# Optimization experiments

Hardware: AMD Instinct MI355X
Metric: run time of the kernel (lower is better)

Reference implementation:

```python
import jax, jax.numpy as jnp
import numpy as np

N, D_FEAT, D, H, L = 2048, 128, 256, 8, 2
DH = D // H
E = 65536
NUM_EDGE_TYPES = 8
MAX_DIST = 10
MAX_DEGREE = 512
D_FF = 4 * D
D_OUT = 128
EPS = 1e-5


def _layernorm(x, g, b):
    mu = jnp.mean(x, axis=-1, keepdims=True)
    var = jnp.mean(jnp.square(x - mu), axis=-1, keepdims=True)
    return (x - mu) * jax.lax.rsqrt(var + EPS) * g + b


def setup_inputs() -> dict:
    key = jax.random.key(0)
    ks = jax.random.split(key, 32)
    inp = {
        "x": jax.random.normal(ks[0], (N, D_FEAT), dtype=jnp.float32),
        "edge_index": jax.random.randint(ks[1], (2, E), 0, N),
        "edge_types": jax.random.randint(ks[2], (E,), 0, NUM_EDGE_TYPES),
        "pos_encoding": jax.random.uniform(ks[3], (N, N), dtype=jnp.float32),
    }
    def xavier(k, shape):
        fan_in, fan_out = shape[0], shape[1]
        lim = float(np.sqrt(6.0 / (fan_in + fan_out)))
        return jax.random.uniform(k, shape, jnp.float32, -lim, lim)
    inp["W_emb"] = xavier(ks[4], (D_FEAT, D)); inp["b_emb"] = jnp.zeros((D,), jnp.float32)
    # stacked per-layer params, stored as [in, out] so y = x @ W + b
    inp["Wq"] = jnp.stack([xavier(jax.random.fold_in(ks[5], l), (D, D)) for l in range(L)])
    inp["Wk"] = jnp.stack([xavier(jax.random.fold_in(ks[6], l), (D, D)) for l in range(L)])
    inp["Wv"] = jnp.stack([xavier(jax.random.fold_in(ks[7], l), (D, D)) for l in range(L)])
    inp["Wo"] = jnp.stack([xavier(jax.random.fold_in(ks[8], l), (D, D)) for l in range(L)])
    for nm in ("bq", "bk", "bv", "bo"):
        inp[nm] = jnp.zeros((L, D), jnp.float32)
    inp["spd_table"] = 0.02 * jax.random.normal(ks[9], (L, MAX_DIST + 1, H), dtype=jnp.float32)
    inp["edge_table"] = 0.02 * jax.random.normal(ks[10], (L, NUM_EDGE_TYPES, H), dtype=jnp.float32)
    inp["din_emb"] = 0.02 * jax.random.normal(ks[11], (L, MAX_DEGREE + 1, D), dtype=jnp.float32)
    inp["dout_emb"] = 0.02 * jax.random.normal(ks[12], (L, MAX_DEGREE + 1, D), dtype=jnp.float32)
    inp["ln1_g"] = jnp.ones((L, D), jnp.float32); inp["ln1_b"] = jnp.zeros((L, D), jnp.float32)
    inp["ln2_g"] = jnp.ones((L, D), jnp.float32); inp["ln2_b"] = jnp.zeros((L, D), jnp.float32)
    inp["W1"] = jnp.stack([xavier(jax.random.fold_in(ks[13], l), (D, D_FF)) for l in range(L)])
    inp["b1"] = jnp.zeros((L, D_FF), jnp.float32)
    inp["W2"] = jnp.stack([xavier(jax.random.fold_in(ks[14], l), (D_FF, D)) for l in range(L)])
    inp["b2"] = jnp.zeros((L, D), jnp.float32)
    inp["W_out"] = xavier(ks[15], (D, D_OUT)); inp["b_out"] = jnp.zeros((D_OUT,), jnp.float32)
    return inp


def _forward(x, edge_index, edge_types, pos_encoding,
             W_emb, b_emb, Wq, bq, Wk, bk, Wv, bv, Wo, bo,
             spd_table, edge_table, din_emb, dout_emb,
             ln1_g, ln1_b, ln2_g, ln2_b, W1, b1, W2, b2, W_out, b_out):
    src, dst = edge_index[0], edge_index[1]
    ones = jnp.ones((E,), jnp.int32)
    deg_out = jnp.clip(jax.ops.segment_sum(ones, src, num_segments=N), 0, MAX_DEGREE)
    deg_in = jnp.clip(jax.ops.segment_sum(ones, dst, num_segments=N), 0, MAX_DEGREE)
    # SPD bucket matrix [N, N] (int), shared across layers
    spd_bucket = jnp.clip(pos_encoding[:, :N] * MAX_DIST + 0.5, 0, MAX_DIST).astype(jnp.int32)

    h = x @ W_emb + b_emb  # node embedding; dropout=0 (eval)
    scale = 1.0 / np.sqrt(DH)
    for l in range(L):
        # centrality encoding
        h = h + din_emb[l][deg_in] + dout_emb[l][deg_out]
        xn = _layernorm(h, ln1_g[l], ln1_b[l])
        q = (xn @ Wq[l] + bq[l]).reshape(N, H, DH).transpose(1, 0, 2)  # [H,N,DH]
        k = (xn @ Wk[l] + bk[l]).reshape(N, H, DH).transpose(1, 0, 2)
        v = (xn @ Wv[l] + bv[l]).reshape(N, H, DH).transpose(1, 0, 2)
        # attention bias [H, N, N]: SPD table gather + per-edge scatter-add
        bias = spd_table[l][spd_bucket].transpose(2, 0, 1)
        e_bias = edge_table[l][edge_types]  # [E, H]
        bias = bias.at[:, src, dst].add(e_bias.T)
        scores = jnp.einsum('hnd,hmd->hnm', q, k) * scale + bias
        attn = jax.nn.softmax(scores, axis=-1)
        attn_out = jnp.einsum('hnm,hmd->hnd', attn, v).transpose(1, 0, 2).reshape(N, D)
        h = h + attn_out @ Wo[l] + bo[l]
        y = _layernorm(h, ln2_g[l], ln2_b[l])
        y = jax.nn.gelu(y @ W1[l] + b1[l], approximate=False) @ W2[l] + b2[l]
        h = h + y
    return h @ W_out + b_out


def reference(x, edge_index, edge_types, pos_encoding,
              W_emb, b_emb, Wq, bq, Wk, bk, Wv, bv, Wo, bo,
              spd_table, edge_table, din_emb, dout_emb,
              ln1_g, ln1_b, ln2_g, ln2_b, W1, b1, W2, b2, W_out, b_out):
    return _forward(x, edge_index, edge_types, pos_encoding,
                    W_emb, b_emb, Wq, bq, Wk, bk, Wv, bv, Wo, bo,
                    spd_table, edge_table, din_emb, dout_emb,
                    ln1_g, ln1_b, ln2_g, ln2_b, W1, b1, W2, b2, W_out, b_out)
```

## Files before the change

kernel.cpp:

```cpp
#include <hip/hip_runtime.h>
#include <math.h>

#define N_NODES 2048
#define D_MODEL 256
#define D_FEAT 128
#define NHEAD 8
#define DH 32
#define NLAYER 2
#define NEDGE 65536
#define D_FF 1024
#define D_OUT 128
#define MAXDEG 512
#define JSPLIT 4

typedef __attribute__((ext_vector_type(8))) short short8;
typedef __attribute__((ext_vector_type(4))) float f32x4;
typedef __attribute__((ext_vector_type(4))) unsigned short u16x4;

__device__ __forceinline__ unsigned short f2bf(float f) {
    unsigned u = __float_as_uint(f);
    unsigned r = (u + 0x7FFFu + ((u >> 16) & 1u)) >> 16;
    return (unsigned short)r;
}

template <int CTRL>
__device__ __forceinline__ float dpp_ror(float x) {
    return __int_as_float(__builtin_amdgcn_update_dpp(0, __float_as_int(x), CTRL, 0xf, 0xf, false));
}

__device__ __forceinline__ void wt_tile(const float* __restrict__ W, unsigned short* __restrict__ Wt,
                                        int K, int Nc, int n0, int k0, int tid,
                                        unsigned short (*tile)[33]) {
    int r = tid >> 3, cg = (tid & 7) * 4;
    float4 w4 = *(const float4*)&W[(size_t)(k0 + r) * Nc + n0 + cg];
    tile[r][cg + 0] = f2bf(w4.x); tile[r][cg + 1] = f2bf(w4.y);
    tile[r][cg + 2] = f2bf(w4.z); tile[r][cg + 3] = f2bf(w4.w);
    __syncthreads();
    int c = tid >> 3, rg = (tid & 7) * 4;
    u16x4 o;
    #pragma unroll
    for (int j = 0; j < 4; j++) o[j] = tile[rg + j][c];
    *(u16x4*)&Wt[(size_t)(n0 + c) * K + k0 + rg] = o;
}

__global__ void mega_prep_kernel(const float* __restrict__ pos, unsigned char* __restrict__ bucket,
                                 unsigned* __restrict__ hist, int* __restrict__ deg_out,
                                 int* __restrict__ deg_in,
                                 const float* __restrict__ Wq, const float* __restrict__ Wk,
                                 const float* __restrict__ Wv, const float* __restrict__ Wo,
                                 const float* __restrict__ W1, const float* __restrict__ W2,
                                 const float* __restrict__ W_emb, const float* __restrict__ W_out,
                                 const float* __restrict__ bq, const float* __restrict__ bk,
                                 const float* __restrict__ bv,
                                 unsigned short* __restrict__ qkvt, unsigned short* __restrict__ wot,
                                 unsigned short* __restrict__ w1t, unsigned short* __restrict__ w2t,
                                 unsigned short* __restrict__ wembt, unsigned short* __restrict__ woutt,
                                 float* __restrict__ bqkv) {
    __shared__ unsigned short tile[32][33];
    int b = blockIdx.x, tid = threadIdx.x;
    if (b < 4096) {
        int i = b * 256 + tid;
        float4 p = *(const float4*)&pos[(size_t)i * 4];
        unsigned b0 = (unsigned)fminf(fmaxf(p.x * 10.f + 0.5f, 0.f), 10.f);
        unsigned b1 = (unsigned)fminf(fmaxf(p.y * 10.f + 0.5f, 0.f), 10.f);
        unsigned b2 = (unsigned)fminf(fmaxf(p.z * 10.f + 0.5f, 0.f), 10.f);
        unsigned b3 = (unsigned)fminf(fmaxf(p.w * 10.f + 0.5f, 0.f), 10.f);
        ((unsigned*)bucket)[i] = b0 | (b1 << 8) | (b2 << 16) | (b3 << 24);
        if (b < 64) {
            #pragma unroll
            for (int k = 0; k < 4; k++) hist[b * 1024 + k * 256 + tid] = 0;
        } else if (b == 64) {
            #pragma unroll
            for (int k = 0; k < 8; k++) deg_out[k * 256 + tid] = 0;
            #pragma unroll
            for (int k = 0; k < 8; k++) deg_in[k * 256 + tid] = 0;
        }
        return;
    }
    int bb = b - 4096;
    if (bb < 512) {
        int z = bb >> 6, t = bb & 63;
        int l = z >> 2, which = z & 3;
        const float* W = (which == 0 ? Wq : which == 1 ? Wk : which == 2 ? Wv : Wo) + (size_t)l * 65536;
        unsigned short* dst = (which < 3) ? qkvt + (size_t)l * 196608 + which * 65536
                                          : wot + (size_t)l * 65536;
        wt_tile(W, dst, 256, 256, (t & 7) * 32, (t >> 3) * 32, tid, tile);
    } else if (bb < 1024) {
        int b2 = bb - 512, l = b2 >> 8, t = b2 & 255;
        wt_tile(W1 + (size_t)l * D_MODEL * D_FF, w1t + (size_t)l * D_MODEL * D_FF,
                D_MODEL, D_FF, (t & 31) * 32, (t >> 5) * 32, tid, tile);
    } else if (bb < 1536) {
        int b3 = bb - 1024, l = b3 >> 8, t = b3 & 255;
        wt_tile(W2 + (size_t)l * D_FF * D_MODEL, w2t + (size_t)l * D_FF * D_MODEL,
                D_FF, D_MODEL, (t & 7) * 32, (t >> 3) * 32, tid, tile);
    } else if (bb < 1568) {
        int b4 = bb - 1536;
        wt_tile(W_emb, wembt, D_FEAT, D_MODEL, (b4 & 7) * 32, (b4 >> 3) * 32, tid, tile);
    } else if (bb < 1600) {
        int b5 = bb - 1568;
        wt_tile(W_out, woutt, D_MODEL, D_OUT, (b5 & 3) * 32, (b5 >> 2) * 32, tid, tile);
    } else {
        int i = (bb - 1600) * 256 + tid;
        if (i < NLAYER * 768) {
            int l = i / 768, j = i % 768;
            const float* src = j < 256 ? bq : j < 512 ? bk : bv;
            bqkv[i] = src[l * 256 + (j & 255)];
        }
    }
}

__global__ void degree_hist_kernel(const int* __restrict__ ei,
                                   int* __restrict__ deg_out, int* __restrict__ deg_in,
                                   unsigned* __restrict__ hist) {
    int e = blockIdx.x * 256 + threadIdx.x;
    if (e < NEDGE) {
        int src = ei[e], dst = ei[NEDGE + e];
        atomicAdd(&deg_out[src], 1);
        atomicAdd(&deg_in[dst], 1);
        atomicAdd(&hist[(src >> 6) * 2048 + dst], 1);
    }
}

__global__ void edge_scan1_kernel(const unsigned* __restrict__ hist,
                                  unsigned* __restrict__ offsets, unsigned* __restrict__ blocksum) {
    __shared__ unsigned tmp[256];
    int t = threadIdx.x;
    int g = blockIdx.x * 256 + t;
    unsigned v = hist[g];
    tmp[t] = v; __syncthreads();
    for (int off = 1; off < 256; off <<= 1) {
        unsigned u = (t >= off) ? tmp[t - off] : 0;
        __syncthreads();
        tmp[t] += u;
        __syncthreads();
    }
    offsets[g] = tmp[t] - v;
    if (t == 255) blocksum[blockIdx.x] = tmp[255];
}

__global__ void edge_scan2_kernel(unsigned* __restrict__ blocksum) {
    __shared__ unsigned tmp[256];
    int t = threadIdx.x;
    unsigned v = blocksum[t];
    tmp[t] = v; __syncthreads();
    for (int off = 1; off < 256; off <<= 1) {
        unsigned u = (t >= off) ? tmp[t - off] : 0;
        __syncthreads();
        tmp[t] += u;
        __syncthreads();
    }
    blocksum[t] = tmp[t] - v;
}

__global__ void edge_scan3_kernel(const unsigned* __restrict__ blocksum,
                                  unsigned* __restrict__ offsets, unsigned* __restrict__ cursor) {
    int g = blockIdx.x * 256 + threadIdx.x;
    unsigned o = offsets[g] + blocksum[blockIdx.x];
    offsets[g] = o; cursor[g] = o;
    if (g == 0) offsets[65536] = NEDGE;
}

__global__ void edge_scatter_kernel(const int* __restrict__ ei, const int* __restrict__ etypes,
                                    unsigned* __restrict__ cursor, unsigned* __restrict__ packed) {
    int e = blockIdx.x * 256 + threadIdx.x;
    if (e < NEDGE) {
        int src = ei[e], dst = ei[NEDGE + e];
        int key = (src >> 6) * 2048 + dst;
        unsigned pos = atomicAdd(&cursor[key], 1);
        packed[pos] = (unsigned)dst | ((unsigned)(src & 63) << 11) | ((unsigned)etypes[e] << 17);
    }
}

__global__ void centrality_ln_kernel(float* __restrict__ h,
                                     const float* __restrict__ din_l,
                                     const float* __restrict__ dout_l,
                                     const int* __restrict__ deg_in,
                                     const int* __restrict__ deg_out,
                                     const float* __restrict__ g,
                                     const float* __restrict__ b,
                                     unsigned short* __restrict__ y) {
    int row = blockIdx.x;
    int tid = threadIdx.x;
    int di = min(max(deg_in[row], 0), MAXDEG);
    int dn = min(max(deg_out[row], 0), MAXDEG);
    float v = h[row * D_MODEL + tid] + din_l[di * D_MODEL + tid] + dout_l[dn * D_MODEL + tid];
    h[row * D_MODEL + tid] = v;
    __shared__ float red[256];
    red[tid] = v; __syncthreads();
    for (int s = 128; s > 0; s >>= 1) { if (tid < s) red[tid] += red[tid + s]; __syncthreads(); }
    float mu = red[0] * (1.0f / D_MODEL);
    __syncthreads();
    float d = v - mu;
    red[tid] = d * d; __syncthreads();
    for (int s = 128; s > 0; s >>= 1) { if (tid < s) red[tid] += red[tid + s]; __syncthreads(); }
    float rstd = rsqrtf(red[0] * (1.0f / D_MODEL) + 1e-5f);
    y[row * D_MODEL + tid] = f2bf(d * rstd * g[tid] + b[tid]);
}

__global__ void layernorm_kernel(const float* __restrict__ x,
                                 const float* __restrict__ g,
                                 const float* __restrict__ b,
                                 unsigned short* __restrict__ y) {
    int row = blockIdx.x;
    int tid = threadIdx.x;
    float v = x[row * D_MODEL + tid];
    __shared__ float red[256];
    red[tid] = v; __syncthreads();
    for (int s = 128; s > 0; s >>= 1) { if (tid < s) red[tid] += red[tid + s]; __syncthreads(); }
    float mu = red[0] * (1.0f / D_MODEL);
    __syncthreads();
    float d = v - mu;
    red[tid] = d * d; __syncthreads();
    for (int s = 128; s > 0; s >>= 1) { if (tid < s) red[tid] += red[tid + s]; __syncthreads(); }
    float rstd = rsqrtf(red[0] * (1.0f / D_MODEL) + 1e-5f);
    y[row * D_MODEL + tid] = f2bf(d * rstd * g[tid] + b[tid]);
}

__global__ void vbt_t_kernel(const unsigned short* __restrict__ qkvb,
                             unsigned short* __restrict__ vbt) {
    __shared__ unsigned short tile[32][33];
    int c0 = blockIdx.x * 32, r0 = blockIdx.y * 32;
    int tid = threadIdx.x;
    int r = tid >> 3, cg = (tid & 7) * 4;
    u16x4 v4 = *(const u16x4*)&qkvb[(size_t)(r0 + r) * 768 + 512 + c0 + cg];
    tile[r][cg + 0] = v4[0]; tile[r][cg + 1] = v4[1];
    tile[r][cg + 2] = v4[2]; tile[r][cg + 3] = v4[3];
    __syncthreads();
    int c = tid >> 3, rg = (tid & 7) * 4;
    u16x4 o;
    #pragma unroll
    for (int j = 0; j < 4; j++) o[j] = tile[rg + j][c];
    *(u16x4*)&vbt[(size_t)(c0 + c) * N_NODES + r0 + rg] = o;
}

template <int ACT, bool RESID, bool OUTBF16, bool AFP32>
__global__ void gemm_mfma_kernel(const void* __restrict__ Av,
                                 const unsigned short* __restrict__ Wt,
                                 const float* __restrict__ bias,
                                 float* __restrict__ C, unsigned short* __restrict__ Cb,
                                 int Nc, int K) {
    __shared__ __align__(16) unsigned short As[32][72];
    __shared__ __align__(16) unsigned short Bs[64][72];
    const unsigned short* A16 = (const unsigned short*)Av;
    const float* A32 = (const float*)Av;
    int tid = threadIdx.x;
    int m0 = blockIdx.y * 32, n0 = blockIdx.x * 64;
    int w = tid >> 6, lane = tid & 63;
    int rg = (w & 1) * 16, cg = (w >> 1) * 32;
    int m = lane & 15, quad = lane >> 4;
    f32x4 acc[2] = {{0.f, 0.f, 0.f, 0.f}, {0.f, 0.f, 0.f, 0.f}};
    int ar = tid >> 3, ac = (tid & 7) * 8;
    uint4 ra; float4 fa0, fa1; uint4 rb0, rb1;
    if (AFP32) {
        fa0 = *(const float4*)&A32[(size_t)(m0 + ar) * K + ac];
        fa1 = *(const float4*)&A32[(size_t)(m0 + ar) * K + ac + 4];
    } else {
        ra = *(const uint4*)&A16[(size_t)(m0 + ar) * K + ac];
    }
    rb0 = *(const uint4*)&Wt[(size_t)(n0 + ar) * K + ac];
    rb1 = *(const uint4*)&Wt[(size_t)(n0 + 32 + ar) * K + ac];
    for (int k0 = 0; k0 < K; k0 += 64) {
        if (AFP32) {
            u16x4 t0 = {f2bf(fa0.x), f2bf(fa0.y), f2bf(fa0.z), f2bf(fa0.w)};
            u16x4 t1 = {f2bf(fa1.x), f2bf(fa1.y), f2bf(fa1.z), f2bf(fa1.w)};
            *(u16x4*)&As[ar][ac] = t0;
            *(u16x4*)&As[ar][ac + 4] = t1;
        } else {
            *(uint4*)&As[ar][ac] = ra;
        }
        *(uint4*)&Bs[ar][ac] = rb0;
        *(uint4*)&Bs[ar + 32][ac] = rb1;
        __syncthreads();
        int kn = k0 + 64;
        if (kn < K) {
            if (AFP32) {
                fa0 = *(const float4*)&A32[(size_t)(m0 + ar) * K + kn + ac];
                fa1 = *(const float4*)&A32[(size_t)(m0 + ar) * K + kn + ac + 4];
            } else {
                ra = *(const uint4*)&A16[(size_t)(m0 + ar) * K + kn + ac];
            }
            rb0 = *(const uint4*)&Wt[(size_t)(n0 + ar) * K + kn + ac];
            rb1 = *(const uint4*)&Wt[(size_t)(n0 + 32 + ar) * K + kn + ac];
        }
        #pragma unroll
        for (int ks = 0; ks < 2; ks++) {
            short8 a = *(const short8*)&As[rg + m][ks * 32 + quad * 8];
            #pragma unroll
            for (int t = 0; t < 2; t++) {
                short8 b = *(const short8*)&Bs[cg + t * 16 + m][ks * 32 + quad * 8];
                acc[t] = __builtin_amdgcn_mfma_f32_16x16x32_bf16(a, b, acc[t], 0, 0, 0);
            }
        }
        __syncthreads();
    }
    #pragma unroll
    for (int t = 0; t < 2; t++) {
        #pragma unroll
        for (int reg = 0; reg < 4; reg++) {
            int row = m0 + rg + quad * 4 + reg;
            int col = n0 + cg + t * 16 + m;
            float val = acc[t][reg] + bias[col];
            if (ACT == 1) val = val * 0.5f * (1.0f + erff(val * 0.7071067811865476f));
            size_t idx = (size_t)row * Nc + col;
            if (RESID) val += C[idx];
            if (OUTBF16) Cb[idx] = f2bf(val);
            else C[idx] = val;
        }
    }
}

__global__ void gemm_oproj_kernel(const float* __restrict__ part_O,
                                  const float* __restrict__ l_part,
                                  const unsigned short* __restrict__ Wt,
                                  const float* __restrict__ bias,
                                  float* __restrict__ C) {
    __shared__ __align__(16) unsigned short As[32][72];
    __shared__ __align__(16) unsigned short Bs[64][72];
    int tid = threadIdx.x;
    int m0 = blockIdx.y * 32, n0 = blockIdx.x * 64;
    int w = tid >> 6, lane = tid & 63;
    int rg = (w & 1) * 16, cg = (w >> 1) * 32;
    int m = lane & 15, quad = lane >> 4;
    f32x4 acc[2] = {{0.f, 0.f, 0.f, 0.f}, {0.f, 0.f, 0.f, 0.f}};
    int ar = tid >> 3, ac = (tid & 7) * 8;
    int row = m0 + ar;
    for (int k0 = 0; k0 < D_MODEL; k0 += 64) {
        int col = k0 + ac;
        int hh = col >> 5;
        float L = 0.f;
        float o[8] = {0.f, 0.f, 0.f, 0.f, 0.f, 0.f, 0.f, 0.f};
        #pragma unroll
        for (int js = 0; js < JSPLIT; js++) {
            L += l_part[((size_t)js * NHEAD + hh) * N_NODES + row];
            const float* pp = &part_O[((size_t)js * N_NODES + row) * D_MODEL + col];
            float4 p0 = *(const float4*)pp;
            float4 p1 = *(const float4*)(pp + 4);
            o[0] += p0.x; o[1] += p0.y; o[2] += p0.z; o[3] += p0.w;
            o[4] += p1.x; o[5] += p1.y; o[6] += p1.z; o[7] += p1.w;
        }
        float inv = 1.0f / L;
        u16x4 t0, t1;
        #pragma unroll
        for (int j = 0; j < 4; j++) { t0[j] = f2bf(o[j] * inv); t1[j] = f2bf(o[j + 4] * inv); }
        *(u16x4*)&As[ar][ac] = t0;
        *(u16x4*)&As[ar][ac + 4] = t1;
        *(uint4*)&Bs[ar][ac] = *(const uint4*)&Wt[(size_t)(n0 + ar) * D_MODEL + k0 + ac];
        *(uint4*)&Bs[ar + 32][ac] = *(const uint4*)&Wt[(size_t)(n0 + 32 + ar) * D_MODEL + k0 + ac];
        __syncthreads();
        #pragma unroll
        for (int ks = 0; ks < 2; ks++) {
            short8 a = *(const short8*)&As[rg + m][ks * 32 + quad * 8];
            #pragma unroll
            for (int t = 0; t < 2; t++) {
                short8 b = *(const short8*)&Bs[cg + t * 16 + m][ks * 32 + quad * 8];
                acc[t] = __builtin_amdgcn_mfma_f32_16x16x32_bf16(a, b, acc[t], 0, 0, 0);
            }
        }
        __syncthreads();
    }
    #pragma unroll
    for (int t = 0; t < 2; t++) {
        #pragma unroll
        for (int reg = 0; reg < 4; reg++) {
            int orow = m0 + rg + quad * 4 + reg;
            int ocol = n0 + cg + t * 16 + m;
            size_t idx = (size_t)orow * D_MODEL + ocol;
            C[idx] += acc[t][reg] + bias[ocol];
        }
    }
}

template <int ACT>
__global__ void gemm64_kernel(const unsigned short* __restrict__ A,
                              const unsigned short* __restrict__ Wt,
                              const float* __restrict__ bias,
                              unsigned short* __restrict__ Cb,
                              int Nc, int K) {
    __shared__ __align__(16) unsigned short As[64][72];
    __shared__ __align__(16) unsigned short Bs[64][72];
    int tid = threadIdx.x;
    int m0 = blockIdx.y * 64, n0 = blockIdx.x * 64;
    int w = tid >> 6, lane = tid & 63;
    int wr = (w & 1) * 32, wc = (w >> 1) * 32;
    int m = lane & 15, quad = lane >> 4;
    f32x4 acc[2][2] = {{{0.f,0.f,0.f,0.f},{0.f,0.f,0.f,0.f}},{{0.f,0.f,0.f,0.f},{0.f,0.f,0.f,0.f}}};
    int sr = tid >> 2, sg = (tid & 3) * 16;
    uint4 a0 = *(const uint4*)&A[(size_t)(m0 + sr) * K + sg];
    uint4 a1 = *(const uint4*)&A[(size_t)(m0 + sr) * K + sg + 8];
    uint4 b0 = *(const uint4*)&Wt[(size_t)(n0 + sr) * K + sg];
    uint4 b1 = *(const uint4*)&Wt[(size_t)(n0 + sr) * K + sg + 8];
    for (int k0 = 0; k0 < K; k0 += 64) {
        *(uint4*)&As[sr][sg] = a0;
        *(uint4*)&As[sr][sg + 8] = a1;
        *(uint4*)&Bs[sr][sg] = b0;
        *(uint4*)&Bs[sr][sg + 8] = b1;
        __syncthreads();
        int kn = k0 + 64;
        if (kn < K) {
            a0 = *(const uint4*)&A[(size_t)(m0 + sr) * K + kn + sg];
            a1 = *(const uint4*)&A[(size_t)(m0 + sr) * K + kn + sg + 8];
            b0 = *(const uint4*)&Wt[(size_t)(n0 + sr) * K + kn + sg];
            b1 = *(const uint4*)&Wt[(size_t)(n0 + sr) * K + kn + sg + 8];
        }
        #pragma unroll
        for (int kh = 0; kh < 2; kh++) {
            short8 x0 = *(const short8*)&As[wr + m][kh * 32 + quad * 8];
            short8 x1 = *(const short8*)&As[wr + 16 + m][kh * 32 + quad * 8];
            short8 y0 = *(const short8*)&Bs[wc + m][kh * 32 + quad * 8];
            short8 y1 = *(const short8*)&Bs[wc + 16 + m][kh * 32 + quad * 8];
            acc[0][0] = __builtin_amdgcn_mfma_f32_16x16x32_bf16(x0, y0, acc[0][0], 0, 0, 0);
            acc[0][1] = __builtin_amdgcn_mfma_f32_16x16x32_bf16(x0, y1, acc[0][1], 0, 0, 0);
            acc[1][0] = __builtin_amdgcn_mfma_f32_16x16x32_bf16(x1, y0, acc[1][0], 0, 0, 0);
            acc[1][1] = __builtin_amdgcn_mfma_f32_16x16x32_bf16(x1, y1, acc[1][1], 0, 0, 0);
        }
        __syncthreads();
    }
    #pragma unroll
    for (int mt = 0; mt < 2; mt++) {
        #pragma unroll
        for (int nt = 0; nt < 2; nt++) {
            #pragma unroll
            for (int reg = 0; reg < 4; reg++) {
                int row = m0 + wr + mt * 16 + quad * 4 + reg;
                int col = n0 + wc + nt * 16 + m;
                float val = acc[mt][nt][reg] + bias[col];
                if (ACT == 1) val = val * 0.5f * (1.0f + erff(val * 0.7071067811865476f));
                Cb[(size_t)row * Nc + col] = f2bf(val);
            }
        }
    }
}

__global__ __launch_bounds__(256)
void flash_attn_kernel(const unsigned short* __restrict__ qkvb,
                       const unsigned short* __restrict__ vbt,
                       const unsigned char* __restrict__ bucket,
                       const float* __restrict__ spd_l,
                       const float* __restrict__ et_l,
                       const unsigned* __restrict__ offsets,
                       const unsigned* __restrict__ packed,
                       float* __restrict__ part_O,
                       float* __restrict__ l_part) {
    __shared__ __align__(16) unsigned short ks[64][40];
    __shared__ __align__(16) unsigned short vs[32][72];
    __shared__ __align__(16) float ov[64][68];
    __shared__ float et[8];

    int tid = threadIdx.x;
    int rb = blockIdx.x;
    int i0 = rb * 64;
    int hh = blockIdx.y;
    int js = blockIdx.z;
    int lane = tid & 63;
    if (tid < 8) et[tid] = et_l[tid * NHEAD + hh];
    float spd_reg = spd_l[(lane < 11 ? lane : 10) * NHEAD + hh];

    int w = tid >> 6;
    int m = lane & 15, quad = lane >> 4;
    int r0 = w * 16;
    short8 aq = *(const short8*)&qkvb[(size_t)(i0 + r0 + m) * 768 + hh * DH + quad * 8];
    float l_st[4] = {0.f, 0.f, 0.f, 0.f};
    f32x4 oacc[2] = {{0.f, 0.f, 0.f, 0.f}, {0.f, 0.f, 0.f, 0.f}};
    const float scale = 0.17677669529663687f;

    int krow = tid >> 2, kcol = (tid & 3) * 8;
    int vrow = tid >> 3, vcol = (tid & 7) * 8;
    int brow = tid >> 2, bcol = (tid & 3) * 16;

    for (int jt = 0; jt < N_NODES / JSPLIT / 64; jt++) {
        int j0 = js * (N_NODES / JSPLIT) + jt * 64;
        __syncthreads();
        *(uint4*)&ks[krow][kcol] =
            *(const uint4*)&qkvb[(size_t)(j0 + krow) * 768 + 256 + hh * DH + kcol];
        *(uint4*)&vs[vrow][vcol] =
            *(const uint4*)&vbt[(size_t)(hh * DH + vrow) * N_NODES + j0 + vcol];
        {
            uint4 b16 = *(const uint4*)&bucket[(size_t)(i0 + brow) * N_NODES + j0 + bcol];
            const unsigned char* bb = (const unsigned char*)&b16;
            float fb[16];
            #pragma unroll
            for (int i = 0; i < 16; i++)
                fb[i] = __int_as_float(
                    __builtin_amdgcn_ds_bpermute(((int)bb[i]) << 2, __float_as_int(spd_reg)));
            #pragma unroll
            for (int g = 0; g < 4; g++) {
                f32x4 st = {fb[g * 4], fb[g * 4 + 1], fb[g * 4 + 2], fb[g * 4 + 3]};
                *(f32x4*)&ov[brow][bcol + g * 4] = st;
            }
        }
        __syncthreads();
        {
            unsigned key0 = (unsigned)rb * 2048 + j0;
            unsigned start = offsets[key0], end = offsets[key0 + 64];
            for (unsigned i = start + tid; i < end; i += 256) {
                unsigned p = packed[i];
                atomicAdd(&ov[(p >> 11) & 63][(p & 2047) - j0], et[(p >> 17) & 7]);
            }
        }
        __syncthreads();
        float sv[4][4];
        #pragma unroll
        for (int t = 0; t < 4; t++) {
            short8 bk8 = *(const short8*)&ks[t * 16 + m][quad * 8];
            f32x4 z = {0.f, 0.f, 0.f, 0.f};
            f32x4 sacc = __builtin_amdgcn_mfma_f32_16x16x32_bf16(aq, bk8, z, 0, 0, 0);
            #pragma unroll
            for (int r = 0; r < 4; r++)
                sv[t][r] = __expf(sacc[r] * scale + ov[r0 + quad * 4 + r][t * 16 + m]);
        }
        #pragma unroll
        for (int r = 0; r < 4; r++) {
            float ps = sv[0][r] + sv[1][r] + sv[2][r] + sv[3][r];
            ps += dpp_ror<0x121>(ps);
            ps += dpp_ror<0x122>(ps);
            ps += dpp_ror<0x124>(ps);
            ps += dpp_ror<0x128>(ps);
            l_st[r] += ps;
        }
        #pragma unroll
        for (int t = 0; t < 4; t++)
            #pragma unroll
            for (int r = 0; r < 4; r++)
                ov[r0 + quad * 4 + r][t * 16 + m] = sv[t][r];
        __builtin_amdgcn_s_waitcnt(0xC07F);
        #pragma unroll
        for (int kh = 0; kh < 2; kh++) {
            f32x4 p0 = *(const f32x4*)&ov[r0 + m][kh * 32 + quad * 8];
            f32x4 p1 = *(const f32x4*)&ov[r0 + m][kh * 32 + quad * 8 + 4];
            short8 pa;
            pa[0] = (short)f2bf(p0[0]); pa[1] = (short)f2bf(p0[1]);
            pa[2] = (short)f2bf(p0[2]); pa[3] = (short)f2bf(p0[3]);
            pa[4] = (short)f2bf(p1[0]); pa[5] = (short)f2bf(p1[1]);
            pa[6] = (short)f2bf(p1[2]); pa[7] = (short)f2bf(p1[3]);
            #pragma unroll
            for (int t = 0; t < 2; t++) {
                short8 vb = *(const short8*)&vs[t * 16 + m][kh * 32 + quad * 8];
                oacc[t] = __builtin_amdgcn_mfma_f32_16x16x32_bf16(pa, vb, oacc[t], 0, 0, 0);
            }
        }
    }
    #pragma unroll
    for (int t = 0; t < 2; t++)
        #pragma unroll
        for (int r = 0; r < 4; r++)
            part_O[((size_t)js * N_NODES + i0 + r0 + quad * 4 + r) * D_MODEL + hh * DH + t * 16 + m] =
                oacc[t][r];
    if (m == 0) {
        #pragma unroll
        for (int r = 0; r < 4; r++) {
            int row = i0 + r0 + quad * 4 + r;
            l_part[((size_t)js * NHEAD + hh) * N_NODES + row] = l_st[r];
        }
    }
}

#define WS_ALLOC(type, name, count) \
    type* name = (type*)base; base += (((size_t)(count) * sizeof(type)) + 255) & ~(size_t)255;

extern "C" void kernel_launch(void* const* d_in, const int* in_sizes, int n_in,
                              void* d_out, int out_size, void* d_ws, size_t ws_size,
                              hipStream_t stream) {
    const float* x          = (const float*)d_in[0];
    const int*   edge_index = (const int*)d_in[1];
    const int*   edge_types = (const int*)d_in[2];
    const float* pos        = (const float*)d_in[3];
    const float* W_emb      = (const float*)d_in[4];
    const float* b_emb      = (const float*)d_in[5];
    const float* Wq         = (const float*)d_in[6];
    const float* Wk         = (const float*)d_in[7];
    const float* Wv         = (const float*)d_in[8];
    const float* Wo         = (const float*)d_in[9];
    const float* bq         = (const float*)d_in[10];
    const float* bk         = (const float*)d_in[11];
    const float* bv         = (const float*)d_in[12];
    const float* bo         = (const float*)d_in[13];
    const float* spd_table  = (const float*)d_in[14];
    const float* edge_table = (const float*)d_in[15];
    const float* din_emb    = (const float*)d_in[16];
    const float* dout_emb   = (const float*)d_in[17];
    const float* ln1_g      = (const float*)d_in[18];
    const float* ln1_b      = (const float*)d_in[19];
    const float* ln2_g      = (const float*)d_in[20];
    const float* ln2_b      = (const float*)d_in[21];
    const float* W1         = (const float*)d_in[22];
    const float* b1         = (const float*)d_in[23];
    const float* W2         = (const float*)d_in[24];
    const float* b2         = (const float*)d_in[25];
    const float* W_out      = (const float*)d_in[26];
    const float* b_out      = (const float*)d_in[27];
    float* out = (float*)d_out;

    char* base = (char*)d_ws;
    WS_ALLOC(int, deg_out, N_NODES)
    WS_ALLOC(int, deg_in, N_NODES)
    WS_ALLOC(float, h, N_NODES * D_MODEL)
    WS_ALLOC(unsigned short, xb, N_NODES * D_MODEL)
    WS_ALLOC(unsigned short, qkvb, N_NODES * 768)
    WS_ALLOC(unsigned short, vbt, D_MODEL * N_NODES)
    WS_ALLOC(unsigned short, ffnb, N_NODES * D_FF)
    WS_ALLOC(unsigned char, bucket, (size_t)N_NODES * N_NODES)
    WS_ALLOC(unsigned short, qkvt, NLAYER * 768 * D_MODEL)
    WS_ALLOC(unsigned short, wot, NLAYER * D_MODEL * D_MODEL)
    WS_ALLOC(unsigned short, w1t, NLAYER * D_MODEL * D_FF)
    WS_ALLOC(unsigned short, w2t, NLAYER * D_FF * D_MODEL)
    WS_ALLOC(unsigned short, wembt, D_FEAT * D_MODEL)
    WS_ALLOC(unsigned short, woutt, D_MODEL * D_OUT)
    WS_ALLOC(float, bqkv, NLAYER * 768)
    WS_ALLOC(unsigned, hist, 65536)
    WS_ALLOC(unsigned, offsets, 65537)
    WS_ALLOC(unsigned, cursor, 65536)
    WS_ALLOC(unsigned, blocksum, 256)
    WS_ALLOC(unsigned, packed, NEDGE)
    WS_ALLOC(float, part_O, (size_t)JSPLIT * N_NODES * D_MODEL)
    WS_ALLOC(float, l_part, (size_t)JSPLIT * NHEAD * N_NODES)

    mega_prep_kernel<<<5702, 256, 0, stream>>>(pos, bucket, hist, deg_out, deg_in,
                                               Wq, Wk, Wv, Wo, W1, W2, W_emb, W_out,
                                               bq, bk, bv, qkvt, wot, w1t, w2t, wembt, woutt, bqkv);
    degree_hist_kernel<<<NEDGE / 256, 256, 0, stream>>>(edge_index, deg_out, deg_in, hist);
    edge_scan1_kernel<<<256, 256, 0, stream>>>(hist, offsets, blocksum);
    edge_scan2_kernel<<<1, 256, 0, stream>>>(blocksum);
    edge_scan3_kernel<<<256, 256, 0, stream>>>(blocksum, offsets, cursor);
    edge_scatter_kernel<<<NEDGE / 256, 256, 0, stream>>>(edge_index, edge_types, cursor, packed);

    gemm_mfma_kernel<0, false, false, true><<<dim3(D_MODEL / 64, N_NODES / 32), 256, 0, stream>>>(
        x, wembt, b_emb, h, nullptr, D_MODEL, D_FEAT);

    for (int l = 0; l < NLAYER; l++) {
        centrality_ln_kernel<<<N_NODES, 256, 0, stream>>>(
            h, din_emb + (size_t)l * (MAXDEG + 1) * D_MODEL,
            dout_emb + (size_t)l * (MAXDEG + 1) * D_MODEL, deg_in, deg_out,
            ln1_g + l * D_MODEL, ln1_b + l * D_MODEL, xb);

        gemm64_kernel<0><<<dim3(768 / 64, N_NODES / 64), 256, 0, stream>>>(
            xb, qkvt + (size_t)l * 768 * D_MODEL, bqkv + l * 768, qkvb, 768, D_MODEL);

        vbt_t_kernel<<<dim3(D_MODEL / 32, N_NODES / 32), 256, 0, stream>>>(qkvb, vbt);

        flash_attn_kernel<<<dim3(N_NODES / 64, NHEAD, JSPLIT), 256, 0, stream>>>(
            qkvb, vbt, bucket, spd_table + (size_t)l * 11 * NHEAD,
            edge_table + (size_t)l * 8 * NHEAD, offsets, packed, part_O, l_part);

        gemm_oproj_kernel<<<dim3(D_MODEL / 64, N_NODES / 32), 256, 0, stream>>>(
            part_O, l_part, wot + (size_t)l * D_MODEL * D_MODEL, bo + l * D_MODEL, h);

        layernorm_kernel<<<N_NODES, 256, 0, stream>>>(h, ln2_g + l * D_MODEL, ln2_b + l * D_MODEL, xb);

        gemm64_kernel<1><<<dim3(D_FF / 64, N_NODES / 64), 256, 0, stream>>>(
            xb, w1t + (size_t)l * D_MODEL * D_FF, b1 + l * D_FF, ffnb, D_FF, D_MODEL);

        gemm_mfma_kernel<0, true, false, false><<<dim3(D_MODEL / 64, N_NODES / 32), 256, 0, stream>>>(
            ffnb, w2t + (size_t)l * D_FF * D_MODEL, b2 + l * D_MODEL, h, nullptr, D_MODEL, D_FF);
    }

    gemm_mfma_kernel<0, false, false, true><<<dim3(D_OUT / 64, N_NODES / 32), 256, 0, stream>>>(
        h, woutt, b_out, out, nullptr, D_OUT, D_MODEL);
}
```

Measured before the change: 301.6 us.

## Replace three-kernel edge scan with atomic allocator; fuse V transpose into QKV GEMM

```diff
diff --git a/kernel.cpp b/kernel.cpp
--- a/kernel.cpp
+++ b/kernel.cpp
@@ -45,7 +45,7 @@
 
 __global__ void mega_prep_kernel(const float* __restrict__ pos, unsigned char* __restrict__ bucket,
                                  unsigned* __restrict__ hist, int* __restrict__ deg_out,
-                                 int* __restrict__ deg_in,
+                                 int* __restrict__ deg_in, unsigned* __restrict__ gcursor,
                                  const float* __restrict__ Wq, const float* __restrict__ Wk,
                                  const float* __restrict__ Wv, const float* __restrict__ Wo,
                                  const float* __restrict__ W1, const float* __restrict__ W2,
@@ -74,6 +74,7 @@
             for (int k = 0; k < 8; k++) deg_out[k * 256 + tid] = 0;
             #pragma unroll
             for (int k = 0; k < 8; k++) deg_in[k * 256 + tid] = 0;
+            if (tid == 0) *gcursor = 0;
         }
         return;
     }
@@ -121,43 +122,26 @@
     }
 }
 
-__global__ void edge_scan1_kernel(const unsigned* __restrict__ hist,
-                                  unsigned* __restrict__ offsets, unsigned* __restrict__ blocksum) {
-    __shared__ unsigned tmp[256];
+__global__ void edge_alloc_kernel(const unsigned* __restrict__ hist,
+                                  unsigned* __restrict__ offsets, unsigned* __restrict__ cursor,
+                                  unsigned* __restrict__ gend, unsigned* __restrict__ gcursor) {
+    int g = blockIdx.x;
     int t = threadIdx.x;
-    int g = blockIdx.x * 256 + t;
-    unsigned v = hist[g];
-    tmp[t] = v; __syncthreads();
-    for (int off = 1; off < 256; off <<= 1) {
-        unsigned u = (t >= off) ? tmp[t - off] : 0;
-        __syncthreads();
-        tmp[t] += u;
-        __syncthreads();
-    }
-    offsets[g] = tmp[t] - v;
-    if (t == 255) blocksum[blockIdx.x] = tmp[255];
-}
-
-__global__ void edge_scan2_kernel(unsigned* __restrict__ blocksum) {
-    __shared__ unsigned tmp[256];
-    int t = threadIdx.x;
-    unsigned v = blocksum[t];
-    tmp[t] = v; __syncthreads();
-    for (int off = 1; off < 256; off <<= 1) {
-        unsigned u = (t >= off) ? tmp[t - off] : 0;
-        __syncthreads();
-        tmp[t] += u;
-        __syncthreads();
-    }
-    blocksum[t] = tmp[t] - v;
-}
-
-__global__ void edge_scan3_kernel(const unsigned* __restrict__ blocksum,
-                                  unsigned* __restrict__ offsets, unsigned* __restrict__ cursor) {
-    int g = blockIdx.x * 256 + threadIdx.x;
-    unsigned o = offsets[g] + blocksum[blockIdx.x];
-    offsets[g] = o; cursor[g] = o;
-    if (g == 0) offsets[65536] = NEDGE;
+    unsigned v = hist[g * 64 + t];
+    unsigned inc = v;
+    #pragma unroll
+    for (int off = 1; off < 64; off <<= 1) {
+        unsigned u = __shfl_up(inc, off);
+        if (t >= off) inc += u;
+    }
+    unsigned total = __shfl(inc, 63);
+    unsigned base = 0;
+    if (t == 63) base = atomicAdd(gcursor, total);
+    base = __shfl(base, 63);
+    unsigned o = base + inc - v;
+    offsets[g * 64 + t] = o;
+    cursor[g * 64 + t] = o;
+    if (t == 63) gend[g] = base + total;
 }
 
 __global__ void edge_scatter_kernel(const int* __restrict__ ei, const int* __restrict__ etypes,
@@ -216,23 +200,6 @@
     y[row * D_MODEL + tid] = f2bf(d * rstd * g[tid] + b[tid]);
 }
 
-__global__ void vbt_t_kernel(const unsigned short* __restrict__ qkvb,
-                             unsigned short* __restrict__ vbt) {
-    __shared__ unsigned short tile[32][33];
-    int c0 = blockIdx.x * 32, r0 = blockIdx.y * 32;
-    int tid = threadIdx.x;
-    int r = tid >> 3, cg = (tid & 7) * 4;
-    u16x4 v4 = *(const u16x4*)&qkvb[(size_t)(r0 + r) * 768 + 512 + c0 + cg];
-    tile[r][cg + 0] = v4[0]; tile[r][cg + 1] = v4[1];
-    tile[r][cg + 2] = v4[2]; tile[r][cg + 3] = v4[3];
-    __syncthreads();
-    int c = tid >> 3, rg = (tid & 7) * 4;
-    u16x4 o;
-    #pragma unroll
-    for (int j = 0; j < 4; j++) o[j] = tile[rg + j][c];
-    *(u16x4*)&vbt[(size_t)(c0 + c) * N_NODES + r0 + rg] = o;
-}
-
 template <int ACT, bool RESID, bool OUTBF16, bool AFP32>
 __global__ void gemm_mfma_kernel(const void* __restrict__ Av,
                                  const unsigned short* __restrict__ Wt,
@@ -370,11 +337,12 @@
     }
 }
 
-template <int ACT>
+template <int ACT, bool VOUT>
 __global__ void gemm64_kernel(const unsigned short* __restrict__ A,
                               const unsigned short* __restrict__ Wt,
                               const float* __restrict__ bias,
                               unsigned short* __restrict__ Cb,
+                              unsigned short* __restrict__ vbt,
                               int Nc, int K) {
     __shared__ __align__(16) unsigned short As[64][72];
     __shared__ __align__(16) unsigned short Bs[64][72];
@@ -415,6 +383,22 @@
         }
         __syncthreads();
     }
+    if (VOUT && n0 >= 512) {
+        #pragma unroll
+        for (int mt = 0; mt < 2; mt++) {
+            #pragma unroll
+            for (int nt = 0; nt < 2; nt++) {
+                int row0 = m0 + wr + mt * 16 + quad * 4;
+                int col = n0 + wc + nt * 16 + m;
+                float bcol = bias[col];
+                u16x4 tv;
+                #pragma unroll
+                for (int reg = 0; reg < 4; reg++) tv[reg] = f2bf(acc[mt][nt][reg] + bcol);
+                *(u16x4*)&vbt[(size_t)(col - 512) * N_NODES + row0] = tv;
+            }
+        }
+        return;
+    }
     #pragma unroll
     for (int mt = 0; mt < 2; mt++) {
         #pragma unroll
@@ -438,6 +422,7 @@
                        const float* __restrict__ spd_l,
                        const float* __restrict__ et_l,
                        const unsigned* __restrict__ offsets,
+                       const unsigned* __restrict__ gend,
                        const unsigned* __restrict__ packed,
                        float* __restrict__ part_O,
                        float* __restrict__ l_part) {
@@ -491,7 +476,7 @@
         __syncthreads();
         {
             unsigned key0 = (unsigned)rb * 2048 + j0;
-            unsigned start = offsets[key0], end = offsets[key0 + 64];
+            unsigned start = offsets[key0], end = gend[key0 >> 6];
             for (unsigned i = start + tid; i < end; i += 256) {
                 unsigned p = packed[i];
                 atomicAdd(&ov[(p >> 11) & 63][(p & 2047) - j0], et[(p >> 17) & 7]);
@@ -607,20 +592,19 @@
     WS_ALLOC(unsigned short, woutt, D_MODEL * D_OUT)
     WS_ALLOC(float, bqkv, NLAYER * 768)
     WS_ALLOC(unsigned, hist, 65536)
-    WS_ALLOC(unsigned, offsets, 65537)
+    WS_ALLOC(unsigned, offsets, 65536)
     WS_ALLOC(unsigned, cursor, 65536)
-    WS_ALLOC(unsigned, blocksum, 256)
+    WS_ALLOC(unsigned, gend, 1024)
+    WS_ALLOC(unsigned, gcursor, 1)
     WS_ALLOC(unsigned, packed, NEDGE)
     WS_ALLOC(float, part_O, (size_t)JSPLIT * N_NODES * D_MODEL)
     WS_ALLOC(float, l_part, (size_t)JSPLIT * NHEAD * N_NODES)
 
-    mega_prep_kernel<<<5702, 256, 0, stream>>>(pos, bucket, hist, deg_out, deg_in,
+    mega_prep_kernel<<<5702, 256, 0, stream>>>(pos, bucket, hist, deg_out, deg_in, gcursor,
                                                Wq, Wk, Wv, Wo, W1, W2, W_emb, W_out,
                                                bq, bk, bv, qkvt, wot, w1t, w2t, wembt, woutt, bqkv);
     degree_hist_kernel<<<NEDGE / 256, 256, 0, stream>>>(edge_index, deg_out, deg_in, hist);
-    edge_scan1_kernel<<<256, 256, 0, stream>>>(hist, offsets, blocksum);
-    edge_scan2_kernel<<<1, 256, 0, stream>>>(blocksum);
-    edge_scan3_kernel<<<256, 256, 0, stream>>>(blocksum, offsets, cursor);
+    edge_alloc_kernel<<<1024, 64, 0, stream>>>(hist, offsets, cursor, gend, gcursor);
     edge_scatter_kernel<<<NEDGE / 256, 256, 0, stream>>>(edge_index, edge_types, cursor, packed);
 
     gemm_mfma_kernel<0, false, false, true><<<dim3(D_MODEL / 64, N_NODES / 32), 256, 0, stream>>>(
@@ -632,22 +616,20 @@
             dout_emb + (size_t)l * (MAXDEG + 1) * D_MODEL, deg_in, deg_out,
             ln1_g + l * D_MODEL, ln1_b + l * D_MODEL, xb);
 
-        gemm64_kernel<0><<<dim3(768 / 64, N_NODES / 64), 256, 0, stream>>>(
-            xb, qkvt + (size_t)l * 768 * D_MODEL, bqkv + l * 768, qkvb, 768, D_MODEL);
-
-        vbt_t_kernel<<<dim3(D_MODEL / 32, N_NODES / 32), 256, 0, stream>>>(qkvb, vbt);
+        gemm64_kernel<0, true><<<dim3(768 / 64, N_NODES / 64), 256, 0, stream>>>(
+            xb, qkvt + (size_t)l * 768 * D_MODEL, bqkv + l * 768, qkvb, vbt, 768, D_MODEL);
 
         flash_attn_kernel<<<dim3(N_NODES / 64, NHEAD, JSPLIT), 256, 0, stream>>>(
             qkvb, vbt, bucket, spd_table + (size_t)l * 11 * NHEAD,
-            edge_table + (size_t)l * 8 * NHEAD, offsets, packed, part_O, l_part);
+            edge_table + (size_t)l * 8 * NHEAD, offsets, gend, packed, part_O, l_part);
 
         gemm_oproj_kernel<<<dim3(D_MODEL / 64, N_NODES / 32), 256, 0, stream>>>(
             part_O, l_part, wot + (size_t)l * D_MODEL * D_MODEL, bo + l * D_MODEL, h);
 
         layernorm_kernel<<<N_NODES, 256, 0, stream>>>(h, ln2_g + l * D_MODEL, ln2_b + l * D_MODEL, xb);
 
-        gemm64_kernel<1><<<dim3(D_FF / 64, N_NODES / 64), 256, 0, stream>>>(
-            xb, w1t + (size_t)l * D_MODEL * D_FF, b1 + l * D_FF, ffnb, D_FF, D_MODEL);
+        gemm64_kernel<1, false><<<dim3(D_FF / 64, N_NODES / 64), 256, 0, stream>>>(
+            xb, w1t + (size_t)l * D_MODEL * D_FF, b1 + l * D_FF, ffnb, nullptr, D_FF, D_MODEL);
 
         gemm_mfma_kernel<0, true, false, false><<<dim3(D_MODEL / 64, N_NODES / 32), 256, 0, stream>>>(
             ffnb, w2t + (size_t)l * D_FF * D_MODEL, b2 + l * D_MODEL, h, nullptr, D_MODEL, D_FF);
```

Measured after the change: 303.6 us. About the same (+0.6%).
